# Performance work log

Measured on AMD Instinct MI355X. Metric: run time of the kernel, lower is better.

The kernel has to match this reference:

```python
import jax, jax.numpy as jnp
import numpy as np

N_NODES = 20000
N_EDGES = 160000
FEAT = 512
HEADS = 4
NEG_SLOPE = 0.2


def setup_inputs() -> dict:
    key = jax.random.key(0)
    ks = jax.random.split(key, 8)
    s = 1.0 / np.sqrt(FEAT)
    return {
        "x": jax.random.normal(ks[0], (N_NODES, FEAT), dtype=jnp.float32),
        "edge_index": jax.random.randint(ks[1], (2, N_EDGES), 0, N_NODES, dtype=jnp.int32),
        "W_l": jax.random.normal(ks[2], (FEAT, HEADS * FEAT), dtype=jnp.float32) * s,
        "W_r": jax.random.normal(ks[3], (FEAT, HEADS * FEAT), dtype=jnp.float32) * s,
        "att": jax.random.normal(ks[4], (HEADS, FEAT), dtype=jnp.float32) * s,
        "bias": jax.random.normal(ks[5], (FEAT,), dtype=jnp.float32) * 0.01,
        "W_cls": jax.random.normal(ks[6], (FEAT, 2), dtype=jnp.float32) * s,
        "b_cls": jnp.zeros((2,), dtype=jnp.float32),
    }


def reference(x, edge_index, W_l, W_r, att, bias, W_cls, b_cls):
    N = x.shape[0]
    H, C = att.shape
    # PyG GATv2Conv default: add self-loops
    loops = jnp.arange(N, dtype=edge_index.dtype)
    ei = jnp.concatenate([edge_index, jnp.stack([loops, loops])], axis=1)
    src, dst = ei[0], ei[1]  # message j -> i

    xl = (x @ W_l).reshape(N, H, C)  # source transform
    xr = (x @ W_r).reshape(N, H, C)  # target transform

    # GATv2 score: e_ij = att . LeakyReLU(xl_j + xr_i)   -> [E, H]
    u = xl[src] + xr[dst]                      # [E, H, C]
    e = jnp.einsum('ehc,hc->eh', jax.nn.leaky_relu(u, NEG_SLOPE), att)

    # segment softmax over incoming edges of each dst node
    m = jax.ops.segment_max(e, dst, num_segments=N)          # [N, H]
    alpha = jnp.exp(e - m[dst])
    denom = jax.ops.segment_sum(alpha, dst, num_segments=N)  # [N, H]
    alpha = alpha / denom[dst]

    # aggregate: out_i = sum_j alpha_ij * xl_j
    out = jax.ops.segment_sum(alpha[:, :, None] * xl[src], dst, num_segments=N)  # [N,H,C]
    out = out.mean(axis=1) + bias  # concat=False -> mean over heads, then bias

    return out @ W_cls + b_cls  # [N, num_classes]
```

## Files before the change

kernel.cpp:

```cpp
#include <hip/hip_runtime.h>
#include <hip/hip_bf16.h>

#define FEAT    512
#define HEADS   4
#define NEG     0.2f

typedef unsigned int uint;
typedef unsigned short ushort_t;
typedef __attribute__((ext_vector_type(8))) short bf16x8v;
typedef __attribute__((ext_vector_type(4))) float f32x4v;
typedef __attribute__((address_space(3))) uint lds_u32_t;
typedef __attribute__((address_space(1))) const uint g_u32_t;

__device__ inline float bf2f(ushort_t h) { return __uint_as_float(((uint)h) << 16); }
__device__ inline ushort_t f2bf(float f) {
    uint u = __float_as_uint(f);
    u += 0x7fff + ((u >> 16) & 1);
    return (ushort_t)(u >> 16);
}
__device__ inline float2 up2(uint d) {
    return make_float2(__uint_as_float(d << 16), __uint_as_float(d & 0xffff0000u));
}
__device__ inline float2 f2add(float2 a, float2 b) { return make_float2(a.x + b.x, a.y + b.y); }
__device__ inline float2 f2min0(float2 a) { return make_float2(fminf(a.x, 0.f), fminf(a.y, 0.f)); }
__device__ inline float2 f2fma(float2 a, float2 b, float2 c) {
    return make_float2(fmaf(a.x, b.x, c.x), fmaf(a.y, b.y, c.y));
}
__device__ inline float2 f2fmas(float s, float2 b, float2 c) {
    return make_float2(fmaf(s, b.x, c.x), fmaf(s, b.y, c.y));
}

__global__ void probe_dtype(const ushort_t* __restrict__ x, int* flag) {
    int lane = threadIdx.x;
    int hits = 0;
    for (int i = lane; i < 128; i += 64) {
        ushort_t w = x[2 * i];
        uint hb = (w >> 8) & 0x7f;
        hits += (hb >= 0x38 && hb <= 0x42) ? 1 : 0;
    }
    #pragma unroll
    for (int off = 32; off >= 1; off >>= 1) hits += __shfl_xor(hits, off);
    if (lane == 0) *flag = (hits >= 64) ? 1 : 0;
}

__global__ __launch_bounds__(256) void canon_kernel(const void* __restrict__ in,
                                                    ushort_t* __restrict__ outp,
                                                    const int* __restrict__ flag, long long n) {
    long long i0 = ((long long)blockIdx.x * 256 + threadIdx.x) * 8;
    if (i0 + 8 <= n) {
        if (*flag) {
            *(uint4*)&outp[i0] = *(const uint4*)((const ushort_t*)in + i0);
        } else {
            const float* f = (const float*)in + i0;
            float4 a = *(const float4*)f, b = *(const float4*)(f + 4);
            ushort_t o[8] = {f2bf(a.x), f2bf(a.y), f2bf(a.z), f2bf(a.w),
                             f2bf(b.x), f2bf(b.y), f2bf(b.z), f2bf(b.w)};
            *(uint4*)&outp[i0] = *(uint4*)o;
        }
    } else {
        for (long long i = i0; i < n; ++i)
            outp[i] = (*flag) ? ((const ushort_t*)in)[i] : f2bf(((const float*)in)[i]);
    }
}

__global__ void init_deg_kernel(int* deg, int N) {
    int i = blockIdx.x * blockDim.x + threadIdx.x;
    if (i < N) deg[i] = 1;
}

__global__ void hist_kernel(const int* __restrict__ dst, int* deg, int E, int N) {
    int i = blockIdx.x * blockDim.x + threadIdx.x;
    if (i < E) {
        int d = dst[i];
        if ((uint)d < (uint)N) atomicAdd(&deg[d], 1);
    }
}

__global__ __launch_bounds__(256) void scan1(const int* __restrict__ deg, int* __restrict__ part,
                                             int* __restrict__ bsum, int N) {
    __shared__ int tmp[256];
    int b = blockIdx.x, tid = threadIdx.x;
    int i0 = b * 1024 + tid * 4;
    int v[4] = {0, 0, 0, 0};
    if (i0 + 4 <= N) { int4 q = *(const int4*)&deg[i0]; v[0]=q.x; v[1]=q.y; v[2]=q.z; v[3]=q.w; }
    else { for (int j = 0; j < 4; ++j) v[j] = (i0 + j < N) ? deg[i0 + j] : 0; }
    int s0 = v[0], s1 = s0 + v[1], s2 = s1 + v[2], s3 = s2 + v[3];
    tmp[tid] = s3;
    __syncthreads();
    for (int off = 1; off < 256; off <<= 1) {
        int t = (tid >= off) ? tmp[tid - off] : 0;
        __syncthreads();
        tmp[tid] += t;
        __syncthreads();
    }
    int base = tid ? tmp[tid - 1] : 0;
    int e[4] = {base, base + s0, base + s1, base + s2};
    if (i0 + 4 <= N) { *(int4*)&part[i0] = make_int4(e[0], e[1], e[2], e[3]); }
    else { for (int j = 0; j < 4; ++j) if (i0 + j < N) part[i0 + j] = e[j]; }
    if (tid == 255) bsum[b] = tmp[255];
}

__global__ void scan2(int* __restrict__ bsum, int* __restrict__ offsN, int Nb) {
    int lane = threadIdx.x;
    int carry = 0;
    for (int base = 0; base < Nb; base += 64) {
        int idx = base + lane;
        int v = (idx < Nb) ? bsum[idx] : 0;
        int incl = v;
        #pragma unroll
        for (int off = 1; off < 64; off <<= 1) {
            int t = __shfl_up(incl, off);
            if (lane >= off) incl += t;
        }
        if (idx < Nb) bsum[idx] = carry + (incl - v);
        carry += __shfl(incl, 63);
    }
    if (lane == 0) *offsN = carry;
}

__global__ __launch_bounds__(256) void scan3(const int* __restrict__ part, const int* __restrict__ bsum,
                                             int* __restrict__ offsets, int* __restrict__ cursor, int N) {
    int b = blockIdx.x;
    int add = bsum[b];
    int i0 = b * 1024 + threadIdx.x * 4;
    #pragma unroll
    for (int j = 0; j < 4; ++j) {
        int i = i0 + j;
        if (i < N) { int o = part[i] + add; offsets[i] = o; cursor[i] = o; }
    }
}

__global__ void scatter_kernel(const int* __restrict__ src, const int* __restrict__ dst,
                               int* cursor, int* srcs, int E, int N) {
    int i = blockIdx.x * blockDim.x + threadIdx.x;
    if (i >= E + N) return;
    int s, d;
    if (i < E) { s = src[i]; d = dst[i]; }
    else       { s = i - E; d = i - E; }
    if ((uint)d >= (uint)N) return;
    int pos = atomicAdd(&cursor[d], 1);
    if ((uint)pos < (uint)(E + N)) srcs[pos] = s;
}

__global__ __launch_bounds__(256) void transpose_canon(const void* __restrict__ in,
                                                       ushort_t* __restrict__ outp,
                                                       const int* __restrict__ flag,
                                                       int K, int N) {
    __shared__ ushort_t t[64][72];
    int k0 = blockIdx.y * 64, n0 = blockIdx.x * 64;
    int tid = threadIdx.x;
    int r = tid >> 3;
    int c = (tid & 7) * 8;
    int isbf = *flag;
    #pragma unroll
    for (int p = 0; p < 2; ++p) {
        int row = r + p * 32;
        size_t base = (size_t)(k0 + row) * N + n0 + c;
        if (isbf) {
            *(uint4*)&t[row][c] = *(const uint4*)((const ushort_t*)in + base);
        } else {
            const float* f = (const float*)in + base;
            float4 a = *(const float4*)f, b = *(const float4*)(f + 4);
            ushort_t o[8] = {f2bf(a.x), f2bf(a.y), f2bf(a.z), f2bf(a.w),
                             f2bf(b.x), f2bf(b.y), f2bf(b.z), f2bf(b.w)};
            *(uint4*)&t[row][c] = *(uint4*)o;
        }
    }
    __syncthreads();
    #pragma unroll
    for (int p = 0; p < 2; ++p) {
        int row = r + p * 32;
        #pragma unroll
        for (int j = 0; j < 8; ++j)
            outp[(size_t)(n0 + row) * K + k0 + c + j] = t[c + j][row];
    }
}

__global__ __launch_bounds__(256) void gemm128(const ushort_t* __restrict__ A,
                                               const ushort_t* __restrict__ Bt,
                                               ushort_t* __restrict__ C,
                                               int M, int Nn, int K) {
    __shared__ ushort_t As[128 * 32];
    __shared__ ushort_t Bs[128 * 32];
    int tid = threadIdx.x;
    int wave = tid >> 6, lane = tid & 63;
    int row0 = blockIdx.y * 128, col0 = blockIdx.x * 128;
    int wm = (wave >> 1) * 64, wn = (wave & 1) * 64;

    f32x4v acc[4][4];
    #pragma unroll
    for (int i = 0; i < 4; ++i)
        #pragma unroll
        for (int j = 0; j < 4; ++j) acc[i][j] = (f32x4v){0.f, 0.f, 0.f, 0.f};

    int fm = lane & 15, kqi = lane >> 4;
    int kqs = kqi ^ (fm >> 2);

    const ushort_t* srcA[2];
    const ushort_t* srcB[2];
    ushort_t* dstA[2];
    ushort_t* dstB[2];
    #pragma unroll
    for (int i = 0; i < 2; ++i) {
        int p = (wave * 2 + i) * 64 + lane;
        int row = p >> 2;
        int kp = (p & 3) ^ ((row >> 2) & 3);
        int gra = row0 + row; if (gra >= M) gra = M - 1;
        srcA[i] = &A[(size_t)gra * K + kp * 8];
        srcB[i] = &Bt[(size_t)(col0 + row) * K + kp * 8];
        dstA[i] = &As[p * 8];
        dstB[i] = &Bs[p * 8];
    }

    for (int k0 = 0; k0 < K; k0 += 32) {
        #pragma unroll
        for (int i = 0; i < 2; ++i) {
            __builtin_amdgcn_global_load_lds((g_u32_t*)srcA[i], (lds_u32_t*)dstA[i], 16, 0, 0);
            __builtin_amdgcn_global_load_lds((g_u32_t*)srcB[i], (lds_u32_t*)dstB[i], 16, 0, 0);
            srcA[i] += 32; srcB[i] += 32;
        }
        __syncthreads();

        bf16x8v af[4], bfr[4];
        #pragma unroll
        for (int mi = 0; mi < 4; ++mi)
            af[mi] = *(const bf16x8v*)&As[(4 * (wm + mi * 16 + fm) + kqs) * 8];
        #pragma unroll
        for (int nj = 0; nj < 4; ++nj)
            bfr[nj] = *(const bf16x8v*)&Bs[(4 * (wn + nj * 16 + fm) + kqs) * 8];
        #pragma unroll
        for (int mi = 0; mi < 4; ++mi)
            #pragma unroll
            for (int nj = 0; nj < 4; ++nj)
                acc[mi][nj] = __builtin_amdgcn_mfma_f32_16x16x32_bf16(af[mi], bfr[nj], acc[mi][nj], 0, 0, 0);
        __syncthreads();
    }

    int col = lane & 15, rq = (lane >> 4) * 4;
    #pragma unroll
    for (int mi = 0; mi < 4; ++mi) {
        #pragma unroll
        for (int r = 0; r < 4; ++r) {
            int gm = row0 + wm + mi * 16 + rq + r;
            if (gm < M) {
                #pragma unroll
                for (int nj = 0; nj < 4; ++nj)
                    C[(size_t)gm * Nn + col0 + wn + nj * 16 + col] = f2bf(acc[mi][nj][r]);
            }
        }
    }
}

__global__ __launch_bounds__(256) void gat_aggregate(
    const ushort_t* __restrict__ xl, int xl_stride,
    const ushort_t* __restrict__ xr, int xr_stride,
    const int* __restrict__ offsets, const int* __restrict__ srcs,
    const ushort_t* __restrict__ att, const ushort_t* __restrict__ bias,
    const ushort_t* __restrict__ Wc, const ushort_t* __restrict__ bc,
    float* __restrict__ out, int c0, int Cn, int N, int EN) {
    int bn = blockIdx.x;
    if (bn >= Cn) return;
    int n = c0 + bn;
    int tid = threadIdx.x;
    int h = tid >> 6, lane = tid & 63;
    int hoff = h * FEAT + lane * 8;

    __shared__ float sh[HEADS][FEAT];
    __shared__ float r0s[HEADS], r1s[HEADS];

    float2 xrr[4], attr[4];
    { uint4 q = *(const uint4*)&xr[(size_t)bn * xr_stride + hoff];
      xrr[0] = up2(q.x); xrr[1] = up2(q.y); xrr[2] = up2(q.z); xrr[3] = up2(q.w); }
    { uint4 q = *(const uint4*)&att[hoff];
      attr[0] = up2(q.x); attr[1] = up2(q.y); attr[2] = up2(q.z); attr[3] = up2(q.w); }

    int start = offsets[n], end = offsets[n + 1];
    start = max(0, min(start, EN));
    end   = max(start, min(end, EN));
    int deg = end - start;

    int sv = 0;
    if (lane < deg) sv = srcs[start + lane];

    float l = 0.f;
    float2 acc[4] = {{0.f,0.f},{0.f,0.f},{0.f,0.f},{0.f,0.f}};
    const ushort_t* xlh = xl + hoff;
    const float2 cneg = make_float2(NEG - 1.0f, NEG - 1.0f);

    auto body = [&](uint4 q) {
        float2 v[4] = {up2(q.x), up2(q.y), up2(q.z), up2(q.w)};
        float2 p2 = make_float2(0.f, 0.f);
        #pragma unroll
        for (int j = 0; j < 4; ++j) {
            float2 u  = f2add(v[j], xrr[j]);
            float2 lr = f2fma(f2min0(u), cneg, u);
            p2 = f2fma(lr, attr[j], p2);
        }
        float p = p2.x + p2.y;
        #pragma unroll
        for (int off = 32; off >= 1; off >>= 1) p += __shfl_xor(p, off);
        float w = __expf(p);
        l += w;
        #pragma unroll
        for (int j = 0; j < 4; ++j) acc[j] = f2fmas(w, v[j], acc[j]);
    };

    int e = 0;
    for (; e + 2 <= deg; e += 2) {
        int s0 = (e < 64) ? __shfl(sv, e) : srcs[start + e];
        int s1 = (e + 1 < 64) ? __shfl(sv, e + 1) : srcs[start + e + 1];
        if ((uint)s0 >= (uint)N) s0 = 0;
        if ((uint)s1 >= (uint)N) s1 = 0;
        uint4 q0 = *(const uint4*)(xlh + (size_t)s0 * xl_stride);
        uint4 q1 = *(const uint4*)(xlh + (size_t)s1 * xl_stride);
        body(q0);
        body(q1);
    }
    if (e < deg) {
        int s0 = (e < 64) ? __shfl(sv, e) : srcs[start + e];
        if ((uint)s0 >= (uint)N) s0 = 0;
        body(*(const uint4*)(xlh + (size_t)s0 * xl_stride));
    }

    float inv = 0.25f / fmaxf(l, 1e-35f);
    #pragma unroll
    for (int j = 0; j < 4; ++j) {
        sh[h][lane * 8 + 2 * j]     = acc[j].x * inv;
        sh[h][lane * 8 + 2 * j + 1] = acc[j].y * inv;
    }
    __syncthreads();

    float p0 = 0.f, p1 = 0.f;
    for (int c = tid; c < FEAT; c += 256) {
        float f = sh[0][c] + sh[1][c] + sh[2][c] + sh[3][c] + bf2f(bias[c]);
        uint w2 = *(const uint*)&Wc[c * 2];
        p0 = fmaf(f, bf2f((ushort_t)(w2 & 0xffff)), p0);
        p1 = fmaf(f, bf2f((ushort_t)(w2 >> 16)), p1);
    }
    #pragma unroll
    for (int off = 32; off >= 1; off >>= 1) {
        p0 += __shfl_xor(p0, off);
        p1 += __shfl_xor(p1, off);
    }
    if (lane == 0) { r0s[h] = p0; r1s[h] = p1; }
    __syncthreads();
    if (tid == 0) {
        out[(size_t)n * 2 + 0] = r0s[0] + r0s[1] + r0s[2] + r0s[3] + bf2f(bc[0]);
        out[(size_t)n * 2 + 1] = r1s[0] + r1s[1] + r1s[2] + r1s[3] + bf2f(bc[1]);
    }
}

extern "C" void kernel_launch(void* const* d_in, const int* in_sizes, int n_in,
                              void* d_out, int out_size, void* d_ws, size_t ws_size,
                              hipStream_t stream) {
    const void* x    = d_in[0];
    const int*  ei   = (const int*)d_in[1];
    const void* W_l  = d_in[2];
    const void* W_r  = d_in[3];
    const void* att  = d_in[4];
    const void* bias = d_in[5];
    const void* Wc   = d_in[6];
    const void* bc   = d_in[7];
    float* out = (float*)d_out;

    const int N  = in_sizes[0] / FEAT;
    const int E  = in_sizes[1] / 2;
    const int K  = FEAT;
    const int HC = HEADS * FEAT;
    const int EN = E + N;
    const int Nb = (N + 1023) / 1024;

    const int* src = ei;
    const int* dst = ei + E;

    char* base = (char*)d_ws;
    size_t off = 0;
    auto alloc = [&](size_t bytes) -> char* {
        char* p = base + off;
        off = (off + bytes + 255) & ~(size_t)255;
        return p;
    };
    int* flag    = (int*)alloc(4);
    int* offsets = (int*)alloc((size_t)(N + 1) * 4);
    int* cursor  = (int*)alloc((size_t)N * 4);
    int* deg     = (int*)alloc((size_t)N * 4);
    int* part    = (int*)alloc((size_t)N * 4);
    int* bsum    = (int*)alloc((size_t)(Nb + 1) * 4);
    int* srcs    = (int*)alloc((size_t)EN * 4);
    ushort_t* attc  = (ushort_t*)alloc((size_t)HC * 2);
    ushort_t* biasc = (ushort_t*)alloc((size_t)FEAT * 2);
    ushort_t* Wcc   = (ushort_t*)alloc((size_t)FEAT * 2 * 2);
    ushort_t* bcc   = (ushort_t*)alloc(2 * 2);
    ushort_t* xc   = (ushort_t*)alloc((size_t)N * K * 2);
    ushort_t* Wcat = (ushort_t*)alloc((size_t)2 * HC * K * 2);
    size_t fixed = off;

    size_t need_merged = (size_t)N * 2 * HC * 2;
    bool merged = (ws_size >= fixed + need_merged);

    probe_dtype<<<1, 64, 0, stream>>>((const ushort_t*)x, flag);
    long long NX = (long long)N * K;
    canon_kernel<<<(int)((NX + 2047) / 2048), 256, 0, stream>>>(x, xc, flag, NX);
    canon_kernel<<<1, 256, 0, stream>>>(att, attc, flag, HC);
    canon_kernel<<<1, 256, 0, stream>>>(bias, biasc, flag, FEAT);
    canon_kernel<<<1, 256, 0, stream>>>(Wc, Wcc, flag, FEAT * 2);
    canon_kernel<<<1, 256, 0, stream>>>(bc, bcc, flag, 2);

    init_deg_kernel<<<(N + 255) / 256, 256, 0, stream>>>(deg, N);
    hist_kernel<<<(E + 255) / 256, 256, 0, stream>>>(dst, deg, E, N);
    scan1<<<Nb, 256, 0, stream>>>(deg, part, bsum, N);
    scan2<<<1, 64, 0, stream>>>(bsum, &offsets[N], Nb);
    scan3<<<Nb, 256, 0, stream>>>(part, bsum, offsets, cursor, N);
    scatter_kernel<<<(EN + 255) / 256, 256, 0, stream>>>(src, dst, cursor, srcs, E, N);

    dim3 tg(HC / 64, K / 64);
    transpose_canon<<<tg, 256, 0, stream>>>(W_l, Wcat, flag, K, HC);
    transpose_canon<<<tg, 256, 0, stream>>>(W_r, Wcat + (size_t)HC * K, flag, K, HC);

    if (merged) {
        ushort_t* xlr = (ushort_t*)(base + fixed);
        dim3 gg(2 * HC / 128, (N + 127) / 128);
        gemm128<<<gg, 256, 0, stream>>>(xc, Wcat, xlr, N, 2 * HC, K);
        gat_aggregate<<<N, 256, 0, stream>>>(xlr, 2 * HC, xlr + HC, 2 * HC,
                                             offsets, srcs, attc, biasc, Wcc, bcc,
                                             out, 0, N, N, EN);
    } else {
        ushort_t* xl = (ushort_t*)alloc((size_t)N * HC * 2);
        size_t remain = (ws_size > off) ? (ws_size - off) : 0;
        long long Cmax = (long long)(remain / ((size_t)HC * 2));
        int C = (Cmax >= N) ? N : (int)(Cmax & ~63LL);
        if (C < 64) C = 64;
        ushort_t* xrc = (ushort_t*)(base + off);
        ushort_t* Wlt = Wcat;
        ushort_t* Wrt = Wcat + (size_t)HC * K;

        dim3 gl(HC / 128, (N + 127) / 128);
        gemm128<<<gl, 256, 0, stream>>>(xc, Wlt, xl, N, HC, K);
        for (int c0 = 0; c0 < N; c0 += C) {
            int Cn = (N - c0 < C) ? (N - c0) : C;
            dim3 gr(HC / 128, (Cn + 127) / 128);
            gemm128<<<gr, 256, 0, stream>>>(xc + (size_t)c0 * K, Wrt, xrc, Cn, HC, K);
            gat_aggregate<<<Cn, 256, 0, stream>>>(xl, HC, xrc, HC,
                                                  offsets, srcs, attc, biasc, Wcc, bcc,
                                                  out, c0, Cn, N, EN);
        }
    }
}
```

Measured before the change: 368.7 us.

## Widen GEMM K-step, prefetch gather rows, drop redundant canon and init kernels

The GEMM now loads two 32-wide K panels per barrier pair, halving the number of syncs, and removes the LDS XOR swizzle. The aggregation loop prefetches the next pair of source rows before processing the current pair, to hide gather latency. Degree initialization is replaced by a memset plus adding one in the scan, and the x canonicalization is skipped when inputs are already bf16. Removing the swizzle risks LDS bank conflicts on the fragment reads.

Result: faster. 353.9 us (-4.0%).

```diff
diff --git a/kernel.cpp b/kernel.cpp
--- a/kernel.cpp
+++ b/kernel.cpp
@@ -45,10 +45,13 @@
 
 __global__ __launch_bounds__(256) void canon_kernel(const void* __restrict__ in,
                                                     ushort_t* __restrict__ outp,
-                                                    const int* __restrict__ flag, long long n) {
+                                                    const int* __restrict__ flag, long long n,
+                                                    int skip_if_bf16) {
+    int isbf = *flag;
+    if (isbf && skip_if_bf16) return;
     long long i0 = ((long long)blockIdx.x * 256 + threadIdx.x) * 8;
     if (i0 + 8 <= n) {
-        if (*flag) {
+        if (isbf) {
             *(uint4*)&outp[i0] = *(const uint4*)((const ushort_t*)in + i0);
         } else {
             const float* f = (const float*)in + i0;
@@ -59,13 +62,8 @@
         }
     } else {
         for (long long i = i0; i < n; ++i)
-            outp[i] = (*flag) ? ((const ushort_t*)in)[i] : f2bf(((const float*)in)[i]);
-    }
-}
-
-__global__ void init_deg_kernel(int* deg, int N) {
-    int i = blockIdx.x * blockDim.x + threadIdx.x;
-    if (i < N) deg[i] = 1;
+            outp[i] = isbf ? ((const ushort_t*)in)[i] : f2bf(((const float*)in)[i]);
+    }
 }
 
 __global__ void hist_kernel(const int* __restrict__ dst, int* deg, int E, int N) {
@@ -82,8 +80,8 @@
     int b = blockIdx.x, tid = threadIdx.x;
     int i0 = b * 1024 + tid * 4;
     int v[4] = {0, 0, 0, 0};
-    if (i0 + 4 <= N) { int4 q = *(const int4*)&deg[i0]; v[0]=q.x; v[1]=q.y; v[2]=q.z; v[3]=q.w; }
-    else { for (int j = 0; j < 4; ++j) v[j] = (i0 + j < N) ? deg[i0 + j] : 0; }
+    if (i0 + 4 <= N) { int4 q = *(const int4*)&deg[i0]; v[0]=q.x+1; v[1]=q.y+1; v[2]=q.z+1; v[3]=q.w+1; }
+    else { for (int j = 0; j < 4; ++j) v[j] = (i0 + j < N) ? deg[i0 + j] + 1 : 0; }
     int s0 = v[0], s1 = s0 + v[1], s2 = s1 + v[2], s3 = s2 + v[3];
     tmp[tid] = s3;
     __syncthreads();
@@ -176,12 +174,14 @@
     }
 }
 
-__global__ __launch_bounds__(256) void gemm128(const ushort_t* __restrict__ A,
+__global__ __launch_bounds__(256) void gemm128(const ushort_t* A_bf, const ushort_t* A_cv,
+                                               const int* __restrict__ flag,
                                                const ushort_t* __restrict__ Bt,
                                                ushort_t* __restrict__ C,
                                                int M, int Nn, int K) {
-    __shared__ ushort_t As[128 * 32];
-    __shared__ ushort_t Bs[128 * 32];
+    __shared__ ushort_t As[2][128 * 32];
+    __shared__ ushort_t Bs[2][128 * 32];
+    const ushort_t* A = (*flag) ? A_bf : A_cv;
     int tid = threadIdx.x;
     int wave = tid >> 6, lane = tid & 63;
     int row0 = blockIdx.y * 128, col0 = blockIdx.x * 128;
@@ -193,46 +193,47 @@
         #pragma unroll
         for (int j = 0; j < 4; ++j) acc[i][j] = (f32x4v){0.f, 0.f, 0.f, 0.f};
 
-    int fm = lane & 15, kqi = lane >> 4;
-    int kqs = kqi ^ (fm >> 2);
-
-    const ushort_t* srcA[2];
-    const ushort_t* srcB[2];
-    ushort_t* dstA[2];
-    ushort_t* dstB[2];
+    int fm = lane & 15, kq8 = (lane >> 4) * 8;
+
+    const ushort_t* srcA[2]; ushort_t* dstA0[2]; ushort_t* dstA1[2];
+    const ushort_t* srcB[2]; ushort_t* dstB0[2]; ushort_t* dstB1[2];
     #pragma unroll
     for (int i = 0; i < 2; ++i) {
         int p = (wave * 2 + i) * 64 + lane;
-        int row = p >> 2;
-        int kp = (p & 3) ^ ((row >> 2) & 3);
+        int row = p >> 2, kp = p & 3;
         int gra = row0 + row; if (gra >= M) gra = M - 1;
         srcA[i] = &A[(size_t)gra * K + kp * 8];
         srcB[i] = &Bt[(size_t)(col0 + row) * K + kp * 8];
-        dstA[i] = &As[p * 8];
-        dstB[i] = &Bs[p * 8];
-    }
-
-    for (int k0 = 0; k0 < K; k0 += 32) {
+        dstA0[i] = &As[0][p * 8]; dstA1[i] = &As[1][p * 8];
+        dstB0[i] = &Bs[0][p * 8]; dstB1[i] = &Bs[1][p * 8];
+    }
+
+    for (int k0 = 0; k0 < K; k0 += 64) {
         #pragma unroll
         for (int i = 0; i < 2; ++i) {
-            __builtin_amdgcn_global_load_lds((g_u32_t*)srcA[i], (lds_u32_t*)dstA[i], 16, 0, 0);
-            __builtin_amdgcn_global_load_lds((g_u32_t*)srcB[i], (lds_u32_t*)dstB[i], 16, 0, 0);
-            srcA[i] += 32; srcB[i] += 32;
+            __builtin_amdgcn_global_load_lds((g_u32_t*)srcA[i],        (lds_u32_t*)dstA0[i], 16, 0, 0);
+            __builtin_amdgcn_global_load_lds((g_u32_t*)(srcA[i] + 32), (lds_u32_t*)dstA1[i], 16, 0, 0);
+            __builtin_amdgcn_global_load_lds((g_u32_t*)srcB[i],        (lds_u32_t*)dstB0[i], 16, 0, 0);
+            __builtin_amdgcn_global_load_lds((g_u32_t*)(srcB[i] + 32), (lds_u32_t*)dstB1[i], 16, 0, 0);
+            srcA[i] += 64; srcB[i] += 64;
         }
         __syncthreads();
 
-        bf16x8v af[4], bfr[4];
-        #pragma unroll
-        for (int mi = 0; mi < 4; ++mi)
-            af[mi] = *(const bf16x8v*)&As[(4 * (wm + mi * 16 + fm) + kqs) * 8];
-        #pragma unroll
-        for (int nj = 0; nj < 4; ++nj)
-            bfr[nj] = *(const bf16x8v*)&Bs[(4 * (wn + nj * 16 + fm) + kqs) * 8];
-        #pragma unroll
-        for (int mi = 0; mi < 4; ++mi)
+        #pragma unroll
+        for (int panel = 0; panel < 2; ++panel) {
+            bf16x8v af[4], bfr[4];
+            #pragma unroll
+            for (int mi = 0; mi < 4; ++mi)
+                af[mi] = *(const bf16x8v*)&As[panel][(wm + mi * 16 + fm) * 32 + kq8];
             #pragma unroll
             for (int nj = 0; nj < 4; ++nj)
-                acc[mi][nj] = __builtin_amdgcn_mfma_f32_16x16x32_bf16(af[mi], bfr[nj], acc[mi][nj], 0, 0, 0);
+                bfr[nj] = *(const bf16x8v*)&Bs[panel][(wn + nj * 16 + fm) * 32 + kq8];
+            #pragma unroll
+            for (int mi = 0; mi < 4; ++mi)
+                #pragma unroll
+                for (int nj = 0; nj < 4; ++nj)
+                    acc[mi][nj] = __builtin_amdgcn_mfma_f32_16x16x32_bf16(af[mi], bfr[nj], acc[mi][nj], 0, 0, 0);
+        }
         __syncthreads();
     }
 
@@ -287,6 +288,10 @@
     const ushort_t* xlh = xl + hoff;
     const float2 cneg = make_float2(NEG - 1.0f, NEG - 1.0f);
 
+    auto getS = [&](int i) -> int {
+        int s = (i < 64) ? __shfl(sv, i) : srcs[start + i];
+        return ((uint)s >= (uint)N) ? 0 : s;
+    };
     auto body = [&](uint4 q) {
         float2 v[4] = {up2(q.x), up2(q.y), up2(q.z), up2(q.w)};
         float2 p2 = make_float2(0.f, 0.f);
@@ -305,22 +310,25 @@
         for (int j = 0; j < 4; ++j) acc[j] = f2fmas(w, v[j], acc[j]);
     };
 
+    uint4 cur0, cur1;
+    {
+        int s0 = getS(0);
+        int s1 = getS(deg > 1 ? 1 : 0);
+        cur0 = *(const uint4*)(xlh + (size_t)s0 * xl_stride);
+        cur1 = *(const uint4*)(xlh + (size_t)s1 * xl_stride);
+    }
     int e = 0;
-    for (; e + 2 <= deg; e += 2) {
-        int s0 = (e < 64) ? __shfl(sv, e) : srcs[start + e];
-        int s1 = (e + 1 < 64) ? __shfl(sv, e + 1) : srcs[start + e + 1];
-        if ((uint)s0 >= (uint)N) s0 = 0;
-        if ((uint)s1 >= (uint)N) s1 = 0;
-        uint4 q0 = *(const uint4*)(xlh + (size_t)s0 * xl_stride);
-        uint4 q1 = *(const uint4*)(xlh + (size_t)s1 * xl_stride);
-        body(q0);
-        body(q1);
-    }
-    if (e < deg) {
-        int s0 = (e < 64) ? __shfl(sv, e) : srcs[start + e];
-        if ((uint)s0 >= (uint)N) s0 = 0;
-        body(*(const uint4*)(xlh + (size_t)s0 * xl_stride));
-    }
+    for (; e + 2 < deg; e += 2) {
+        int t0 = getS(e + 2);
+        int t1 = getS(e + 3 < deg ? e + 3 : e + 2);
+        uint4 n0 = *(const uint4*)(xlh + (size_t)t0 * xl_stride);
+        uint4 n1 = *(const uint4*)(xlh + (size_t)t1 * xl_stride);
+        body(cur0);
+        body(cur1);
+        cur0 = n0; cur1 = n1;
+    }
+    body(cur0);
+    if (deg - e == 2) body(cur1);
 
     float inv = 0.25f / fmaxf(l, 1e-35f);
     #pragma unroll
@@ -400,13 +408,13 @@
 
     probe_dtype<<<1, 64, 0, stream>>>((const ushort_t*)x, flag);
     long long NX = (long long)N * K;
-    canon_kernel<<<(int)((NX + 2047) / 2048), 256, 0, stream>>>(x, xc, flag, NX);
-    canon_kernel<<<1, 256, 0, stream>>>(att, attc, flag, HC);
-    canon_kernel<<<1, 256, 0, stream>>>(bias, biasc, flag, FEAT);
-    canon_kernel<<<1, 256, 0, stream>>>(Wc, Wcc, flag, FEAT * 2);
-    canon_kernel<<<1, 256, 0, stream>>>(bc, bcc, flag, 2);
-
-    init_deg_kernel<<<(N + 255) / 256, 256, 0, stream>>>(deg, N);
+    canon_kernel<<<(int)((NX + 2047) / 2048), 256, 0, stream>>>(x, xc, flag, NX, 1);
+    canon_kernel<<<1, 256, 0, stream>>>(att, attc, flag, HC, 0);
+    canon_kernel<<<1, 256, 0, stream>>>(bias, biasc, flag, FEAT, 0);
+    canon_kernel<<<1, 256, 0, stream>>>(Wc, Wcc, flag, FEAT * 2, 0);
+    canon_kernel<<<1, 256, 0, stream>>>(bc, bcc, flag, 2, 0);
+
+    hipMemsetAsync(deg, 0, (size_t)N * 4, stream);
     hist_kernel<<<(E + 255) / 256, 256, 0, stream>>>(dst, deg, E, N);
     scan1<<<Nb, 256, 0, stream>>>(deg, part, bsum, N);
     scan2<<<1, 64, 0, stream>>>(bsum, &offsets[N], Nb);
@@ -417,10 +425,12 @@
     transpose_canon<<<tg, 256, 0, stream>>>(W_l, Wcat, flag, K, HC);
     transpose_canon<<<tg, 256, 0, stream>>>(W_r, Wcat + (size_t)HC * K, flag, K, HC);
 
+    const ushort_t* x_bf = (const ushort_t*)x;
+
     if (merged) {
         ushort_t* xlr = (ushort_t*)(base + fixed);
         dim3 gg(2 * HC / 128, (N + 127) / 128);
-        gemm128<<<gg, 256, 0, stream>>>(xc, Wcat, xlr, N, 2 * HC, K);
+        gemm128<<<gg, 256, 0, stream>>>(x_bf, xc, flag, Wcat, xlr, N, 2 * HC, K);
         gat_aggregate<<<N, 256, 0, stream>>>(xlr, 2 * HC, xlr + HC, 2 * HC,
                                              offsets, srcs, attc, biasc, Wcc, bcc,
                                              out, 0, N, N, EN);
@@ -435,11 +445,12 @@
         ushort_t* Wrt = Wcat + (size_t)HC * K;
 
         dim3 gl(HC / 128, (N + 127) / 128);
-        gemm128<<<gl, 256, 0, stream>>>(xc, Wlt, xl, N, HC, K);
+        gemm128<<<gl, 256, 0, stream>>>(x_bf, xc, flag, Wlt, xl, N, HC, K);
         for (int c0 = 0; c0 < N; c0 += C) {
             int Cn = (N - c0 < C) ? (N - c0) : C;
             dim3 gr(HC / 128, (Cn + 127) / 128);
-            gemm128<<<gr, 256, 0, stream>>>(xc + (size_t)c0 * K, Wrt, xrc, Cn, HC, K);
+            gemm128<<<gr, 256, 0, stream>>>(x_bf + (size_t)c0 * K, xc + (size_t)c0 * K, flag,
+                                            Wrt, xrc, Cn, HC, K);
             gat_aggregate<<<Cn, 256, 0, stream>>>(xl, HC, xrc, HC,
                                                   offsets, srcs, attc, biasc, Wcc, bcc,
                                                   out, c0, Cn, N, EN);
```
